# Optimization experiments

Hardware: AMD Instinct MI355X
Metric: run time of the kernel (lower is better)

The kernel has to match this reference:

```python
import jax, jax.numpy as jnp
import numpy as np

K = 2  # kernel_size


def setup_inputs() -> dict:
    key = jax.random.key(0)
    k1, k2, k3, k4, k5 = jax.random.split(key, 5)
    B, C, H, W_sp = 8, 256, 128, 128
    N = 512                      # number of keypoints
    E = C * K * K                # embed_dim = 1024
    img_feat_highres = jax.random.normal(k1, (B, C, H, W_sp), dtype=jnp.float32)
    W = jax.random.normal(k2, (E, C, K, K), dtype=jnp.float32) * 0.02  # conv weight, OIHW
    b = jax.random.normal(k3, (E,), dtype=jnp.float32) * 0.02          # conv bias
    batch_indices = jnp.broadcast_to(jnp.arange(B, dtype=jnp.int64)[:, None], (B, N))
    pixel_x_id = jax.random.randint(k4, (B, N), 0, H // 2, dtype=jnp.int64)  # low-res ids
    pixel_y_id = jax.random.randint(k5, (B, N), 0, H // 2, dtype=jnp.int64)
    return {
        "img_feat_highres": img_feat_highres,
        "W": W,
        "b": b,
        "batch_indices": batch_indices,
        "pixel_x_id": pixel_x_id,
        "pixel_y_id": pixel_y_id,
    }


def reference(img_feat_highres, W, b, batch_indices, pixel_x_id, pixel_y_id):
    # Dense conv2d, stride 1, padding = K-1 (torch nn.Conv2d semantics)
    patches = jax.lax.conv_general_dilated(
        img_feat_highres, W,
        window_strides=(1, 1),
        padding=((K - 1, K - 1), (K - 1, K - 1)),
        dimension_numbers=("NCHW", "OIHW", "NCHW"),
    ) + b[None, :, None, None]  # (B, E, H+K-1, W+K-1)

    y0 = 2 * pixel_y_id  # (B, N)
    x0 = 2 * pixel_x_id

    def samp(dy, dx):
        # advanced indices at dims 0,2,3 (non-adjacent) -> result (B, N, E)
        return patches[batch_indices, :, y0 + dy, x0 + dx]

    local_feat = jnp.concatenate(
        [samp(0, 0), samp(K, 0), samp(0, K), samp(K, K)], axis=2
    )  # (B, N, 4E)
    return jnp.transpose(local_feat, (0, 2, 1))  # (B, 4E, N)
```

## Files before the change

kernel.cpp:

```cpp
#include <hip/hip_runtime.h>
#include <stdint.h>


typedef __attribute__((ext_vector_type(8))) short bf16x8;
typedef __attribute__((ext_vector_type(4))) float f32x4;

#define GAS(p) ((const __attribute__((address_space(1))) void*)(p))
#define LAS(p) ((__attribute__((address_space(3))) void*)(p))

__device__ __forceinline__ unsigned short f2bf(float f) {
    union { float f; uint32_t u; } x; x.f = f;
    uint32_t u = x.u;
    uint32_t r = (u + 0x7FFFu + ((u >> 16) & 1u)) >> 16;
    return (unsigned short)r;
}

__global__ __launch_bounds__(256)
void prep_kernel(const float* __restrict__ img, const float* __restrict__ Wf,
                 unsigned short* __restrict__ Wp, unsigned short* __restrict__ zp,
                 unsigned short* __restrict__ imgT) {
    __shared__ unsigned short sT[8192];
    const int blk = blockIdx.x;
    const int t = threadIdx.x;

    if (blk < 1024) {
        const int e = blk, c = t;
        float4 w4 = *(const float4*)&Wf[(size_t)e * 1024 + c * 4];
        Wp[e * 1024 + 0 * 256 + c] = f2bf(w4.x);
        Wp[e * 1024 + 1 * 256 + c] = f2bf(w4.y);
        Wp[e * 1024 + 2 * 256 + c] = f2bf(w4.z);
        Wp[e * 1024 + 3 * 256 + c] = f2bf(w4.w);
        if (e == 0 && c < 32) {
            uint4 z = {0, 0, 0, 0};
            ((uint4*)zp)[c] = z;
        }
        return;
    }

    const int ib = blk - 1024;
    const int cc = ib & 3;
    const int y  = (ib >> 2) & 127;
    const int b  = ib >> 9;
    const int x  = t & 127;
    const int ah = t >> 7;
    const size_t ibase = ((size_t)b * 256 + cc * 64) * 16384 + (size_t)y * 128 + x;
    #pragma unroll
    for (int it = 0; it < 16; ++it) {
        const int a = ah + 2 * it;
        const float v0 = img[ibase + (size_t)(2 * a)     * 16384];
        const float v1 = img[ibase + (size_t)(2 * a + 1) * 16384];
        const unsigned int pk = (unsigned)f2bf(v0) | ((unsigned)f2bf(v1) << 16);
        *(unsigned int*)&sT[x * 64 + ((2 * a) ^ (2 * (x & 31)))] = pk;
    }
    __syncthreads();
    unsigned short* ob = imgT + (((size_t)b * 128 + y) * 128) * 256 + cc * 64;
    #pragma unroll
    for (int jj = 0; jj < 16; ++jj) {
        const int oo = t + 256 * jj;
        const int xx = oo >> 5;
        const int c2 = oo & 31;
        const unsigned int pk = *(const unsigned int*)&sT[xx * 64 + 2 * (c2 ^ (xx & 31))];
        *(unsigned int*)&ob[(size_t)xx * 256 + c2 * 2] = pk;
    }
}

__global__ __launch_bounds__(256)
void gemm_kernel(const unsigned short* __restrict__ Wp,
                 const unsigned short* __restrict__ imgT,
                 const unsigned short* __restrict__ zp,
                 const int* __restrict__ bidx,
                 const int* __restrict__ pxid,
                 const int* __restrict__ pyid,
                 const float* __restrict__ bias,
                 float* __restrict__ out) {
    const int orig = blockIdx.x;
    const int wg = (orig & 7) * 128 + (orig >> 3);
    const int et = wg & 7;
    const int nt = wg >> 3;
    const int g  = nt >> 2;
    const int n0 = (nt & 3) * 128;
    const int e0 = et * 128;
    const int b = g >> 2, o = g & 3;

    const int tid  = threadIdx.x;
    const int lane = tid & 63;
    const int wid  = tid >> 6;
    const int wr   = wid >> 1;
    const int wc   = wid & 1;

    __shared__ unsigned short sW[128 * 64];
    __shared__ unsigned short sA[128 * 64];

    const int row0 = tid >> 3;
    const int cg   = (tid & 7) ^ (row0 & 7);
    int ay[4], ax[4];
    size_t apl[4];
    #pragma unroll
    for (int r = 0; r < 4; ++r) {
        const int row = row0 + 32 * r;
        const int gi = b * 512 + n0 + row;
        apl[r] = (size_t)bidx[gi] * (128 * 128 * 256);
        ay[r] = 2 * pyid[gi] - 1 + (o & 1) * 2;
        ax[r] = 2 * pxid[gi] - 1 + (o >> 1) * 2;
    }

    const f32x4 fzero = {0.f, 0.f, 0.f, 0.f};
    f32x4 acc[4][4];
    #pragma unroll
    for (int m = 0; m < 4; ++m)
        #pragma unroll
        for (int nf = 0; nf < 4; ++nf) acc[m][nf] = fzero;

    for (int kc = 0; kc < 16; ++kc) {
        if (kc) __syncthreads();
        const int p   = kc >> 2;
        const int csh = (kc & 3) * 64;
        const int y   = 0;
        (void)y;
        #pragma unroll
        for (int r = 0; r < 4; ++r) {
            const int i   = r * 256 + tid;
            const int row = row0 + 32 * r;
            const unsigned short* gw = Wp + (size_t)(e0 + row) * 1024 + kc * 64 + cg * 8;
            __builtin_amdgcn_global_load_lds(GAS(gw), LAS(&sW[i * 8]), 16, 0, 0);
            const int yy = ay[r] + (p >> 1);
            const int xx = ax[r] + (p & 1);
            const unsigned short* ga =
                ((unsigned)yy < 128u && (unsigned)xx < 128u)
                    ? imgT + apl[r] + ((size_t)(yy * 128 + xx)) * 256 + csh + cg * 8
                    : zp + cg * 8;
            __builtin_amdgcn_global_load_lds(GAS(ga), LAS(&sA[i * 8]), 16, 0, 0);
        }
        asm volatile("s_waitcnt vmcnt(0)" ::: "memory");
        __syncthreads();

        #pragma unroll
        for (int ks = 0; ks < 2; ++ks) {
            bf16x8 af[4], bfr[4];
            #pragma unroll
            for (int m = 0; m < 4; ++m) {
                const int row = wr * 64 + m * 16 + (lane & 15);
                const int cl  = (ks * 4 + (lane >> 4)) ^ (row & 7);
                af[m] = *(const bf16x8*)&sW[row * 64 + cl * 8];
            }
            #pragma unroll
            for (int nf = 0; nf < 4; ++nf) {
                const int row = wc * 64 + nf * 16 + (lane & 15);
                const int cl  = (ks * 4 + (lane >> 4)) ^ (row & 7);
                bfr[nf] = *(const bf16x8*)&sA[row * 64 + cl * 8];
            }
            __builtin_amdgcn_s_setprio(1);
            #pragma unroll
            for (int m = 0; m < 4; ++m)
                #pragma unroll
                for (int nf = 0; nf < 4; ++nf)
                    acc[m][nf] = __builtin_amdgcn_mfma_f32_16x16x32_bf16(
                        af[m], bfr[nf], acc[m][nf], 0, 0, 0);
            __builtin_amdgcn_s_setprio(0);
        }
    }

    const int erow_l = (lane >> 4) * 4;
    const int ncol_l = lane & 15;
    #pragma unroll
    for (int m = 0; m < 4; ++m) {
        #pragma unroll
        for (int nf = 0; nf < 4; ++nf) {
            const int nn = n0 + wc * 64 + nf * 16 + ncol_l;
            #pragma unroll
            for (int reg = 0; reg < 4; ++reg) {
                const int e = e0 + wr * 64 + m * 16 + erow_l + reg;
                out[((size_t)g * 1024 + e) * 512 + nn] = acc[m][nf][reg] + bias[e];
            }
        }
    }
}

extern "C" void kernel_launch(void* const* d_in, const int* in_sizes, int n_in,
                              void* d_out, int out_size, void* d_ws, size_t ws_size,
                              hipStream_t stream) {
    const float* img  = (const float*)d_in[0];
    const float* Wf   = (const float*)d_in[1];
    const float* bias = (const float*)d_in[2];
    const int*   bidx = (const int*)d_in[3];
    const int*   pxid = (const int*)d_in[4];
    const int*   pyid = (const int*)d_in[5];
    float* out = (float*)d_out;

    unsigned short* Wp   = (unsigned short*)((char*)d_ws + (32u << 20));
    unsigned short* zp   = (unsigned short*)((char*)d_ws + (36u << 20));
    unsigned short* imgT = (unsigned short*)((char*)d_ws + (64u << 20));

    hipLaunchKernelGGL(prep_kernel, dim3(5120), dim3(256), 0, stream,
                       img, Wf, Wp, zp, imgT);
    hipLaunchKernelGGL(gemm_kernel, dim3(1024), dim3(256), 0, stream,
                       Wp, imgT, zp, bidx, pxid, pyid, bias, out);
}
```

Baseline: 81.67 us.

## Double-buffer GEMM LDS tiles and vectorize image transpose loads

The GEMM kernel now uses two LDS buffers per operand and prefetches two k-chunks ahead. Partial vmcnt waits let global-to-LDS loads overlap MFMA compute instead of draining memory on every iteration. The prep kernel's transpose now reads float4 vectors per thread instead of scalar floats, cutting the number of load instructions. LDS use doubles, which may reduce occupancy, and the partial wait count assumes exactly eight outstanding loads per stage.

```diff
diff --git a/kernel.cpp b/kernel.cpp
--- a/kernel.cpp
+++ b/kernel.cpp
@@ -41,16 +41,23 @@
     const int cc = ib & 3;
     const int y  = (ib >> 2) & 127;
     const int b  = ib >> 9;
-    const int x  = t & 127;
-    const int ah = t >> 7;
-    const size_t ibase = ((size_t)b * 256 + cc * 64) * 16384 + (size_t)y * 128 + x;
-    #pragma unroll
-    for (int it = 0; it < 16; ++it) {
-        const int a = ah + 2 * it;
-        const float v0 = img[ibase + (size_t)(2 * a)     * 16384];
-        const float v1 = img[ibase + (size_t)(2 * a + 1) * 16384];
-        const unsigned int pk = (unsigned)f2bf(v0) | ((unsigned)f2bf(v1) << 16);
-        *(unsigned int*)&sT[x * 64 + ((2 * a) ^ (2 * (x & 31)))] = pk;
+    const int xq = t & 31;
+    const int ch = t >> 5;
+    unsigned int* sU = (unsigned int*)sT;
+    const size_t pl = ((size_t)b * 256 + cc * 64) * 16384 + (size_t)y * 128;
+    #pragma unroll
+    for (int it = 0; it < 4; ++it) {
+        const int cp = it * 8 + ch;
+        const float4 v0 = *(const float4*)&img[pl + (size_t)(2 * cp)     * 16384 + xq * 4];
+        const float4 v1 = *(const float4*)&img[pl + (size_t)(2 * cp + 1) * 16384 + xq * 4];
+        const float a0[4] = {v0.x, v0.y, v0.z, v0.w};
+        const float a1[4] = {v1.x, v1.y, v1.z, v1.w};
+        #pragma unroll
+        for (int j = 0; j < 4; ++j) {
+            const int x = xq * 4 + j;
+            const unsigned int pk = (unsigned)f2bf(a0[j]) | ((unsigned)f2bf(a1[j]) << 16);
+            sU[x * 32 + (cp ^ (x & 31))] = pk;
+        }
     }
     __syncthreads();
     unsigned short* ob = imgT + (((size_t)b * 128 + y) * 128) * 256 + cc * 64;
@@ -59,7 +66,7 @@
         const int oo = t + 256 * jj;
         const int xx = oo >> 5;
         const int c2 = oo & 31;
-        const unsigned int pk = *(const unsigned int*)&sT[xx * 64 + 2 * (c2 ^ (xx & 31))];
+        const unsigned int pk = sU[xx * 32 + (c2 ^ (xx & 31))];
         *(unsigned int*)&ob[(size_t)xx * 256 + c2 * 2] = pk;
     }
 }
@@ -88,8 +95,8 @@
     const int wr   = wid >> 1;
     const int wc   = wid & 1;
 
-    __shared__ unsigned short sW[128 * 64];
-    __shared__ unsigned short sA[128 * 64];
+    __shared__ unsigned short sW[2][8192];
+    __shared__ unsigned short sA[2][8192];
 
     const int row0 = tid >> 3;
     const int cg   = (tid & 7) ^ (row0 & 7);
@@ -111,28 +118,32 @@
         #pragma unroll
         for (int nf = 0; nf < 4; ++nf) acc[m][nf] = fzero;
 
-    for (int kc = 0; kc < 16; ++kc) {
-        if (kc) __syncthreads();
+    auto stage = [&](int kc, int buf) {
         const int p   = kc >> 2;
         const int csh = (kc & 3) * 64;
-        const int y   = 0;
-        (void)y;
         #pragma unroll
         for (int r = 0; r < 4; ++r) {
             const int i   = r * 256 + tid;
             const int row = row0 + 32 * r;
             const unsigned short* gw = Wp + (size_t)(e0 + row) * 1024 + kc * 64 + cg * 8;
-            __builtin_amdgcn_global_load_lds(GAS(gw), LAS(&sW[i * 8]), 16, 0, 0);
+            __builtin_amdgcn_global_load_lds(GAS(gw), LAS(&sW[buf][i * 8]), 16, 0, 0);
             const int yy = ay[r] + (p >> 1);
             const int xx = ax[r] + (p & 1);
             const unsigned short* ga =
                 ((unsigned)yy < 128u && (unsigned)xx < 128u)
                     ? imgT + apl[r] + ((size_t)(yy * 128 + xx)) * 256 + csh + cg * 8
                     : zp + cg * 8;
-            __builtin_amdgcn_global_load_lds(GAS(ga), LAS(&sA[i * 8]), 16, 0, 0);
-        }
-        asm volatile("s_waitcnt vmcnt(0)" ::: "memory");
-        __syncthreads();
+            __builtin_amdgcn_global_load_lds(GAS(ga), LAS(&sA[buf][i * 8]), 16, 0, 0);
+        }
+    };
+
+    stage(0, 0);
+    stage(1, 1);
+    for (int kt = 0; kt < 16; ++kt) {
+        const int cur = kt & 1;
+        if (kt == 15) { asm volatile("s_waitcnt vmcnt(0)" ::: "memory"); }
+        else          { asm volatile("s_waitcnt vmcnt(8)" ::: "memory"); }
+        __builtin_amdgcn_s_barrier();
 
         #pragma unroll
         for (int ks = 0; ks < 2; ++ks) {
@@ -141,13 +152,13 @@
             for (int m = 0; m < 4; ++m) {
                 const int row = wr * 64 + m * 16 + (lane & 15);
                 const int cl  = (ks * 4 + (lane >> 4)) ^ (row & 7);
-                af[m] = *(const bf16x8*)&sW[row * 64 + cl * 8];
+                af[m] = *(const bf16x8*)&sW[cur][row * 64 + cl * 8];
             }
             #pragma unroll
             for (int nf = 0; nf < 4; ++nf) {
                 const int row = wc * 64 + nf * 16 + (lane & 15);
                 const int cl  = (ks * 4 + (lane >> 4)) ^ (row & 7);
-                bfr[nf] = *(const bf16x8*)&sA[row * 64 + cl * 8];
+                bfr[nf] = *(const bf16x8*)&sA[cur][row * 64 + cl * 8];
             }
             __builtin_amdgcn_s_setprio(1);
             #pragma unroll
@@ -158,6 +169,9 @@
                         af[m], bfr[nf], acc[m][nf], 0, 0, 0);
             __builtin_amdgcn_s_setprio(0);
         }
+
+        __builtin_amdgcn_s_barrier();
+        if (kt + 2 < 16) stage(kt + 2, cur);
     }
 
     const int erow_l = (lane >> 4) * 4;
```

Measured after the change: 84.22 us. 1.03x slower.
